# Performance work log

Hardware: AMD Instinct MI355X
Metric: run time of the kernel (lower is better)

## Reference

```python
import math
import jax, jax.numpy as jnp
import numpy as np

B, L, T, D, H, SD = 8, 512, 512, 768, 12, 5


def setup_inputs() -> dict:
    key = jax.random.key(0)
    ks = jax.random.split(key, 16)
    s = 0.02
    return {
        "q": jax.random.normal(ks[0], (B, L, D), jnp.float32),
        "k": jax.random.normal(ks[1], (B, T, D), jnp.float32),
        "v": jax.random.normal(ks[2], (B, T, D), jnp.float32),
        "pairwise_locs": jax.random.normal(ks[3], (B, L, T, SD), jnp.float32),
        "key_padding_mask": jax.random.randint(ks[4], (B, T), 0, 2).astype(bool),
        "Wq": jax.random.normal(ks[5], (D, D), jnp.float32) * s,
        "bq": jnp.zeros((D,), jnp.float32),
        "Wk": jax.random.normal(ks[6], (D, D), jnp.float32) * s,
        "bk": jnp.zeros((D,), jnp.float32),
        "Wv": jax.random.normal(ks[7], (D, D), jnp.float32) * s,
        "bv": jnp.zeros((D,), jnp.float32),
        "Wl": jax.random.normal(ks[8], (D, H * (SD + 1)), jnp.float32) * s,
        "bl": jnp.zeros((H * (SD + 1),), jnp.float32),
        "Wf": jax.random.normal(ks[9], (D, D), jnp.float32) * s,
        "bf": jnp.zeros((D,), jnp.float32),
    }


def reference(q, k, v, pairwise_locs, key_padding_mask,
              Wq, bq, Wk, bk, Wv, bv, Wl, bl, Wf, bf):
    b, l, d = q.shape
    t = k.shape[1]
    sd = pairwise_locs.shape[-1]
    h = Wl.shape[1] // (sd + 1)          # spatial_multihead=True -> h == n_head
    dh = d // h

    # projections -> [h, b, seq, dh]
    qh = (q @ Wq + bq).reshape(b, l, h, dh).transpose(2, 0, 1, 3)
    kh = (k @ Wk + bk).reshape(b, t, h, dh).transpose(2, 0, 1, 3)
    vh = (v @ Wv + bv).reshape(b, t, h, dh).transpose(2, 0, 1, 3)

    attn = jnp.einsum('hblk,hbtk->hblt', qh, kh) / math.sqrt(dh)

    # language-conditioned spatial weights from residual (= q input)
    sw = (q @ Wl + bl).reshape(b, l, h, sd + 1).transpose(2, 0, 1, 3)  # [h,b,l,sd+1]
    spatial_bias = sw[..., :1]
    spatial_w = sw[..., 1:]
    loc_attn = jax.nn.sigmoid(
        jnp.einsum('hbld,bltd->hblt', spatial_w, pairwise_locs) + spatial_bias)

    mask = key_padding_mask[None, :, None, :]          # [1,b,1,t]
    attn = jnp.where(mask, -jnp.inf, attn)
    loc_attn = jnp.where(mask, 0.0, loc_attn)

    fused_attn = jax.nn.softmax(jnp.log(jnp.clip(loc_attn, 1e-6)) + attn, axis=3)

    out = jnp.einsum('hblt,hbtv->hblv', fused_attn, vh)
    out = out.transpose(1, 2, 0, 3).reshape(b, l, d)
    out = out @ Wf + bf
    return (out, fused_attn)
```

## Files before the change

kernel.cpp:

```cpp
#include <hip/hip_runtime.h>
#include <hip/hip_bf16.h>

#define B_ 8
#define L_ 512
#define T_ 512
#define D_ 768
#define H_ 12
#define DH_ 64
#define SD_ 5
#define NSW_ 72
#define K2_ 1536
#define K3_ 2304

typedef __attribute__((ext_vector_type(8))) short bf16x8;
typedef __attribute__((ext_vector_type(4))) float f32x4;
typedef unsigned short ushort_t;

__device__ __forceinline__ unsigned short f2bf(float x) {
    union { __hip_bfloat16 h; unsigned short u; } cv;
    cv.h = __float2bfloat16(x);
    return cv.u;
}
__device__ __forceinline__ float bf2f(unsigned short u) {
    union { unsigned short u; __hip_bfloat16 h; } cv;
    cv.u = u;
    return __bfloat162float(cv.h);
}

__device__ __forceinline__ void gload_lds16(const void* g, void* l) {
    __builtin_amdgcn_global_load_lds((const __attribute__((address_space(1))) void*)g,
                                     (__attribute__((address_space(3))) void*)l,
                                     16, 0, 0);
}

__global__ __launch_bounds__(256) void asplit_kernel(
    const float* __restrict__ q, const float* __restrict__ k, const float* __restrict__ v,
    short* __restrict__ q2, short* __restrict__ k2, short* __restrict__ v2)
{
    const int z = blockIdx.z;
    const float* A = (z == 0) ? q : (z == 1) ? k : v;
    short* O = (z == 0) ? q2 : (z == 1) ? k2 : v2;
    const int col = blockIdx.x * 256 + threadIdx.x;
    const int m   = blockIdx.y;
    if (col >= D_) return;
    const float a = A[(size_t)m * D_ + col];
    const unsigned short hi = f2bf(a);
    const unsigned short lo = f2bf(a - bf2f(hi));
    O[(size_t)m * K2_ + col]       = (short)hi;
    O[(size_t)m * K2_ + D_ + col]  = (short)lo;
}

__global__ __launch_bounds__(256) void wsplit_kernel(
    const float* __restrict__ Wq, const float* __restrict__ Wk,
    const float* __restrict__ Wv, const float* __restrict__ Wl,
    const float* __restrict__ Wf,
    short* __restrict__ WqT3, short* __restrict__ WkT3, short* __restrict__ WvT3,
    short* __restrict__ WlT3, short* __restrict__ WfT3)
{
    const int z = blockIdx.z;
    const float* W; short* O; int Nw, Npad;
    if (z == 0)      { W = Wq; O = WqT3; Nw = D_;   Npad = 768; }
    else if (z == 1) { W = Wk; O = WkT3; Nw = D_;   Npad = 768; }
    else if (z == 2) { W = Wv; O = WvT3; Nw = D_;   Npad = 768; }
    else if (z == 3) { W = Wl; O = WlT3; Nw = NSW_; Npad = 128; }
    else             { W = Wf; O = WfT3; Nw = D_;   Npad = 768; }

    const int k0 = blockIdx.x * 64;
    const int n0 = blockIdx.y * 64;
    if (n0 >= Npad) return;

    __shared__ float sm[64][65];
    const int c  = threadIdx.x & 63;
    const int r4 = threadIdx.x >> 6;

#pragma unroll
    for (int i = 0; i < 16; i++) {
        const int r = i * 4 + r4;
        float val = 0.f;
        if (n0 + c < Nw) val = W[(size_t)(k0 + r) * Nw + n0 + c];
        sm[r][c] = val;
    }
    __syncthreads();

#pragma unroll
    for (int i = 0; i < 16; i++) {
        const int nl = i * 4 + r4;
        const int n  = n0 + nl;
        if (n >= Npad) continue;
        const float v = (n < Nw) ? sm[c][nl] : 0.f;
        const unsigned short hi = f2bf(v);
        const unsigned short lo = f2bf(v - bf2f(hi));
        const size_t rb = (size_t)n * K3_;
        O[rb + k0 + c]        = (short)hi;
        O[rb + 768 + k0 + c]  = (short)lo;
        O[rb + 1536 + k0 + c] = (short)hi;
    }
}

__global__ __launch_bounds__(256) void mfma_gemm(
    const short* __restrict__ q2, const short* __restrict__ k2, const short* __restrict__ v2,
    const short* __restrict__ WqT3, const short* __restrict__ WkT3,
    const short* __restrict__ WvT3, const short* __restrict__ WlT3,
    const short* __restrict__ WfT3,
    const float* __restrict__ bq, const float* __restrict__ bk,
    const float* __restrict__ bv, const float* __restrict__ bl,
    const float* __restrict__ bf,
    const short* __restrict__ outp2,
    ushort_t* __restrict__ qs2a, ushort_t* __restrict__ ks2a, ushort_t* __restrict__ vt2,
    float* __restrict__ swv, float* __restrict__ outf,
    int zoff)
{
    const int z = zoff + blockIdx.z;
    const short* A2; const short* WT3; const float* bias;
    if (z == 0)      { A2 = q2;    WT3 = WqT3; bias = bq; }
    else if (z == 1) { A2 = k2;    WT3 = WkT3; bias = bk; }
    else if (z == 2) { A2 = v2;    WT3 = WvT3; bias = bv; }
    else if (z == 3) { A2 = q2;    WT3 = WlT3; bias = bl; }
    else             { A2 = outp2; WT3 = WfT3; bias = bf; }

    if (z == 3 && blockIdx.x != 0) return;

    const int m0 = blockIdx.y * 128;
    const int n0 = blockIdx.x * 128;

    __shared__ __align__(16) short As[128 * 32];
    __shared__ __align__(16) short Bs[128 * 32];

    const int tid  = threadIdx.x;
    const int lane = tid & 63;
    const int wv_  = tid >> 6;
    const int wm   = (wv_ & 1) << 6;
    const int wn   = (wv_ >> 1) << 6;
    const int l15  = lane & 15;
    const int quad = lane >> 4;

    f32x4 acc[4][4] = {};

    const int sa  = tid;
    const int sb  = tid + 256;
    const int ra  = sa >> 2, ka = (sa & 3) << 3;
    const int rb  = sb >> 2, kb8 = (sb & 3) << 3;

    for (int kb = 0; kb < K3_; kb += 32) {
        const int akb = (kb < 768) ? kb : kb - 768;
        __syncthreads();
        gload_lds16(A2  + (size_t)(m0 + ra) * K2_ + akb + ka,  &As[sa << 3]);
        gload_lds16(A2  + (size_t)(m0 + rb) * K2_ + akb + kb8, &As[sb << 3]);
        gload_lds16(WT3 + (size_t)(n0 + ra) * K3_ + kb  + ka,  &Bs[sa << 3]);
        gload_lds16(WT3 + (size_t)(n0 + rb) * K3_ + kb  + kb8, &Bs[sb << 3]);
        __syncthreads();

        bf16x8 af[4], bfr[4];
#pragma unroll
        for (int t = 0; t < 4; t++) {
            af[t]  = *(const bf16x8*)&As[(wm + t * 16 + l15) * 32 + quad * 8];
            bfr[t] = *(const bf16x8*)&Bs[(wn + t * 16 + l15) * 32 + quad * 8];
        }
#pragma unroll
        for (int mt = 0; mt < 4; mt++)
#pragma unroll
            for (int nt = 0; nt < 4; nt++)
                acc[mt][nt] = __builtin_amdgcn_mfma_f32_16x16x32_bf16(
                    af[mt], bfr[nt], acc[mt][nt], 0, 0, 0);
    }

    if (z <= 2) {
        ushort_t* dst = (z == 0) ? qs2a : (z == 1) ? ks2a : vt2;
#pragma unroll
        for (int nt = 0; nt < 4; nt++) {
            const int col = n0 + wn + nt * 16 + l15;
            const int hh = col >> 6, dd = col & 63;
            const float bvv = bias[col];
#pragma unroll
            for (int mt = 0; mt < 4; mt++) {
                const int rowb = m0 + wm + mt * 16 + quad * 4;
                if (z < 2) {
#pragma unroll
                    for (int r = 0; r < 4; r++) {
                        const int gr = rowb + r;
                        const int bb = gr >> 9, ll = gr & 511;
                        const float x = acc[mt][nt][r] + bvv;
                        const ushort_t hi = f2bf(x);
                        const ushort_t lo = f2bf(x - bf2f(hi));
                        const size_t base = (((size_t)hh * B_ + bb) * 512 + ll) * 128 + dd;
                        dst[base]      = hi;
                        dst[base + 64] = lo;
                    }
                } else {
                    const int bb = rowb >> 9, tt = rowb & 511;
                    ushort_t hi4[4], lo4[4];
#pragma unroll
                    for (int r = 0; r < 4; r++) {
                        const float x = acc[mt][nt][r] + bvv;
                        hi4[r] = f2bf(x);
                        lo4[r] = f2bf(x - bf2f(hi4[r]));
                    }
                    const size_t base = (((size_t)hh * B_ + bb) * 128 + dd) * 512 + tt;
                    *(ushort4*)&dst[base]            = *(ushort4*)hi4;
                    *(ushort4*)&dst[base + 64 * 512] = *(ushort4*)lo4;
                }
            }
        }
    } else if (z == 3) {
#pragma unroll
        for (int nt = 0; nt < 4; nt++) {
            const int col = n0 + wn + nt * 16 + l15;
            if (col >= NSW_) continue;
            const float bvv = bias[col];
#pragma unroll
            for (int mt = 0; mt < 4; mt++) {
                const int row = m0 + wm + mt * 16 + quad * 4;
#pragma unroll
                for (int r = 0; r < 4; r++)
                    swv[(size_t)(row + r) * NSW_ + col] = acc[mt][nt][r] + bvv;
            }
        }
    } else {
#pragma unroll
        for (int nt = 0; nt < 4; nt++) {
            const int col = n0 + wn + nt * 16 + l15;
            const float bvv = bias[col];
#pragma unroll
            for (int mt = 0; mt < 4; mt++) {
                const int row = m0 + wm + mt * 16 + quad * 4;
#pragma unroll
                for (int r = 0; r < 4; r++)
                    outf[(size_t)(row + r) * D_ + col] = acc[mt][nt][r] + bvv;
            }
        }
    }
}

__global__ __launch_bounds__(256) void sig_kernel(
    const float* __restrict__ ploc, const float* __restrict__ swv,
    const int* __restrict__ maskp, _Float16* __restrict__ sig16)
{
    const int b = blockIdx.y;
    const int l = blockIdx.x;
    const int tid = threadIdx.x;

    __shared__ float pls[512 * 5];
    __shared__ float sws[72];
    __shared__ int   msk[512];

    const float* src = ploc + (size_t)(b * 512 + l) * 512 * 5;
    for (int i = tid; i < 640; i += 256)
        *(float4*)&pls[i * 4] = *(const float4*)(src + i * 4);
    if (tid < 72) sws[tid] = swv[(size_t)(b * 512 + l) * NSW_ + tid];
    for (int i = tid; i < 512; i += 256) msk[i] = maskp[b * 512 + i];
    __syncthreads();

    for (int e = tid; e < H_ * 512; e += 256) {
        const int t  = e & 511;
        const int hh = e >> 9;
        float s = sws[hh * 6];
#pragma unroll
        for (int d = 0; d < SD_; d++) s += sws[hh * 6 + 1 + d] * pls[t * 5 + d];
        const float sig = msk[t] ? 0.f : fmaxf(1.f / (1.f + __expf(-s)), 1e-6f);
        sig16[(((size_t)hh * B_ + b) * 512 + l) * 512 + t] = (_Float16)sig;
    }
}

__global__ __launch_bounds__(256) void attn_kernel(
    const ushort_t* __restrict__ qs2, const ushort_t* __restrict__ ks2,
    const ushort_t* __restrict__ vt2, const _Float16* __restrict__ sig16,
    float* __restrict__ fused, ushort_t* __restrict__ outp2,
    float* __restrict__ sums)
{
    const int h  = blockIdx.z;
    const int b  = blockIdx.y;
    const int l0 = blockIdx.x << 6;
    const int hb = h * B_ + b;
    const int tid  = threadIdx.x;
    const int lane = tid & 63;
    const int wv   = tid >> 6;
    const int l15  = lane & 15;
    const int quad = lane >> 4;

    __shared__ __align__(16) ushort_t qs[64 * 128];
    __shared__ __align__(16) ushort_t ks[64 * 128];
    __shared__ __align__(16) ushort_t vts[128 * 64];
    __shared__ __align__(16) ushort_t ps[64 * 136];
    __shared__ float ssb[4 * 64];
    __shared__ float ssum[64];

    {
        const size_t qbase = ((size_t)hb * 512 + l0) * 128;
#pragma unroll
        for (int j = 0; j < 4; j++) {
            const int i = tid + 256 * j;
            const int r = i >> 4, c = i & 15, gc = c ^ (r & 7);
            gload_lds16(qs2 + qbase + r * 128 + gc * 8, &qs[i * 8]);
        }
    }

    float pacc = 0.f;
    f32x4 accpv[4] = {};

    for (int t0 = 0; t0 < T_; t0 += 64) {
        __syncthreads();
        {
            const size_t kbase = ((size_t)hb * 512 + t0) * 128;
#pragma unroll
            for (int j = 0; j < 4; j++) {
                const int i = tid + 256 * j;
                const int r = i >> 4, c = i & 15, gc = c ^ (r & 7);
                gload_lds16(ks2 + kbase + r * 128 + gc * 8, &ks[i * 8]);
            }
            const size_t vbase = (size_t)hb * 128 * 512;
#pragma unroll
            for (int j = 0; j < 4; j++) {
                const int i = tid + 256 * j;
                const int r = i >> 3, c = i & 7, gc = c ^ (r & 7);
                gload_lds16(vt2 + vbase + (size_t)r * 512 + t0 + gc * 8, &vts[i * 8]);
            }
        }
        __syncthreads();

        float sigv[4][4];
        {
            const _Float16* sgp = sig16 + (((size_t)hb * 512 + l0) * 512) + t0 + wv * 16 + l15;
#pragma unroll
            for (int mt = 0; mt < 4; mt++)
#pragma unroll
                for (int r2 = 0; r2 < 4; r2++)
                    sigv[mt][r2] = (float)sgp[(size_t)(mt * 16 + quad * 4 + r2) * 512];
        }

        f32x4 acq[4] = {};
        {
            const int trow = wv * 16 + l15;
            const int tsw  = trow & 7;
            const bf16x8 bk0 = *(const bf16x8*)&ks[trow * 128 + ((0  + quad) ^ tsw) * 8];
            const bf16x8 bk1 = *(const bf16x8*)&ks[trow * 128 + ((4  + quad) ^ tsw) * 8];
            const bf16x8 bk2 = *(const bf16x8*)&ks[trow * 128 + ((8  + quad) ^ tsw) * 8];
            const bf16x8 bk3 = *(const bf16x8*)&ks[trow * 128 + ((12 + quad) ^ tsw) * 8];
#pragma unroll
            for (int mt = 0; mt < 4; mt++) {
                const int arow = mt * 16 + l15;
                const int asw  = arow & 7;
                const bf16x8 a0 = *(const bf16x8*)&qs[arow * 128 + ((0  + quad) ^ asw) * 8];
                const bf16x8 a1 = *(const bf16x8*)&qs[arow * 128 + ((4  + quad) ^ asw) * 8];
                const bf16x8 a2 = *(const bf16x8*)&qs[arow * 128 + ((8  + quad) ^ asw) * 8];
                const bf16x8 a3 = *(const bf16x8*)&qs[arow * 128 + ((12 + quad) ^ asw) * 8];
                f32x4 a = acq[mt];
                a = __builtin_amdgcn_mfma_f32_16x16x32_bf16(a0, bk0, a, 0, 0, 0);
                a = __builtin_amdgcn_mfma_f32_16x16x32_bf16(a1, bk1, a, 0, 0, 0);
                a = __builtin_amdgcn_mfma_f32_16x16x32_bf16(a0, bk2, a, 0, 0, 0);
                a = __builtin_amdgcn_mfma_f32_16x16x32_bf16(a1, bk3, a, 0, 0, 0);
                a = __builtin_amdgcn_mfma_f32_16x16x32_bf16(a2, bk0, a, 0, 0, 0);
                a = __builtin_amdgcn_mfma_f32_16x16x32_bf16(a3, bk1, a, 0, 0, 0);
                acq[mt] = a;
            }
        }

        {
            const int tcol = wv * 16 + l15;
#pragma unroll
            for (int mt = 0; mt < 4; mt++)
#pragma unroll
                for (int r2 = 0; r2 < 4; r2++) {
                    const int lrow = mt * 16 + quad * 4 + r2;
                    const float p  = sigv[mt][r2] * __expf(acq[mt][r2] * 0.125f);
                    const ushort_t hi = f2bf(p);
                    const ushort_t lo = f2bf(p - bf2f(hi));
                    ps[lrow * 136 + tcol]      = hi;
                    ps[lrow * 136 + 64 + tcol] = lo;
                }
        }
        __syncthreads();

        {
            const int row = tid >> 2, c4 = tid & 3;
            float vbuf[16];
            float s = 0.f;
#pragma unroll
            for (int jj = 0; jj < 16; jj++) {
                const int t = c4 * 16 + jj;
                const float pv = bf2f(ps[row * 136 + t]) + bf2f(ps[row * 136 + 64 + t]);
                vbuf[jj] = pv;
                s += pv;
            }
            pacc += s;
            float* dstf = fused + ((size_t)hb * 512 + l0 + row) * 512 + t0 + c4 * 16;
#pragma unroll
            for (int jj = 0; jj < 4; jj++)
                *(float4*)(dstf + jj * 4) = *(float4*)&vbuf[jj * 4];
        }

        {
            const int vrh = wv * 16 + l15;
            const int vrl = 64 + vrh;
            const int swh = vrh & 7, swl = vrl & 7;
            const bf16x8 bh0 = *(const bf16x8*)&vts[vrh * 64 + ((0 + quad) ^ swh) * 8];
            const bf16x8 bh1 = *(const bf16x8*)&vts[vrh * 64 + ((4 + quad) ^ swh) * 8];
            const bf16x8 bl0 = *(const bf16x8*)&vts[vrl * 64 + ((0 + quad) ^ swl) * 8];
            const bf16x8 bl1 = *(const bf16x8*)&vts[vrl * 64 + ((4 + quad) ^ swl) * 8];
#pragma unroll
            for (int mt = 0; mt < 4; mt++) {
                const int prow = mt * 16 + l15;
                const bf16x8 ph0 = *(const bf16x8*)&ps[prow * 136 + 0  + quad * 8];
                const bf16x8 ph1 = *(const bf16x8*)&ps[prow * 136 + 32 + quad * 8];
                const bf16x8 pl0 = *(const bf16x8*)&ps[prow * 136 + 64 + quad * 8];
                const bf16x8 pl1 = *(const bf16x8*)&ps[prow * 136 + 96 + quad * 8];
                f32x4 a = accpv[mt];
                a = __builtin_amdgcn_mfma_f32_16x16x32_bf16(ph0, bh0, a, 0, 0, 0);
                a = __builtin_amdgcn_mfma_f32_16x16x32_bf16(ph1, bh1, a, 0, 0, 0);
                a = __builtin_amdgcn_mfma_f32_16x16x32_bf16(ph0, bl0, a, 0, 0, 0);
                a = __builtin_amdgcn_mfma_f32_16x16x32_bf16(ph1, bl1, a, 0, 0, 0);
                a = __builtin_amdgcn_mfma_f32_16x16x32_bf16(pl0, bh0, a, 0, 0, 0);
                a = __builtin_amdgcn_mfma_f32_16x16x32_bf16(pl1, bh1, a, 0, 0, 0);
                accpv[mt] = a;
            }
        }
    }

    __syncthreads();
    ssb[(tid & 3) * 64 + (tid >> 2)] = pacc;
    __syncthreads();
    if (tid < 64) {
        const float s = ssb[tid] + ssb[64 + tid] + ssb[128 + tid] + ssb[192 + tid];
        ssum[tid] = s;
        sums[(size_t)hb * 512 + l0 + tid] = s;
    }
    __syncthreads();

#pragma unroll
    for (int mt = 0; mt < 4; mt++)
#pragma unroll
        for (int r2 = 0; r2 < 4; r2++) {
            const int lrow = mt * 16 + quad * 4 + r2;
            const float val = accpv[mt][r2] / ssum[lrow];
            const ushort_t hi = f2bf(val);
            const ushort_t lo = f2bf(val - bf2f(hi));
            const size_t obase = ((size_t)(b * 512 + l0 + lrow)) * K2_ + h * 64 + wv * 16 + l15;
            outp2[obase]       = hi;
            outp2[obase + D_]  = lo;
        }
}

__global__ __launch_bounds__(256) void norm_kernel(
    float* __restrict__ fused, const float* __restrict__ sums)
{
    const int gi = blockIdx.x * 256 + threadIdx.x;
    float4* f4 = (float4*)fused;
    float4 v = f4[gi];
    const float inv = 1.f / sums[gi >> 7];
    v.x *= inv; v.y *= inv; v.z *= inv; v.w *= inv;
    f4[gi] = v;
}

extern "C" void kernel_launch(void* const* d_in, const int* in_sizes, int n_in,
                              void* d_out, int out_size, void* d_ws, size_t ws_size,
                              hipStream_t stream) {
    const float* q    = (const float*)d_in[0];
    const float* k    = (const float*)d_in[1];
    const float* v    = (const float*)d_in[2];
    const float* ploc = (const float*)d_in[3];
    const int*   mask = (const int*)  d_in[4];
    const float* Wq   = (const float*)d_in[5];
    const float* bq   = (const float*)d_in[6];
    const float* Wk   = (const float*)d_in[7];
    const float* bk   = (const float*)d_in[8];
    const float* Wv   = (const float*)d_in[9];
    const float* bv   = (const float*)d_in[10];
    const float* Wl   = (const float*)d_in[11];
    const float* bl   = (const float*)d_in[12];
    const float* Wf   = (const float*)d_in[13];
    const float* bf   = (const float*)d_in[14];

    char* base = (char*)d_ws;
    short*    q2    = (short*)(base + 0);
    short*    k2    = (short*)(base + 12582912);
    short*    v2    = (short*)(base + 25165824);
    short*    WqT3  = (short*)(base + 37748736);
    short*    WkT3  = (short*)(base + 41287680);
    short*    WvT3  = (short*)(base + 44826624);
    short*    WlT3  = (short*)(base + 48365568);
    _Float16* sig16 = (_Float16*)(base + 0);
    short*    WfT3  = (short*)(base + 50331648);
    ushort_t* qs2a  = (ushort_t*)(base + 53870592);
    ushort_t* ks2a  = (ushort_t*)(base + 66453504);
    ushort_t* vt2   = (ushort_t*)(base + 79036416);
    float*    swv   = (float*)(base + 91619328);
    float*    sums  = (float*)(base + 92798976);
    short*    outp2 = (short*)(base + 92995584);

    float* out   = (float*)d_out;
    float* fused = out + (size_t)4096 * D_;

    asplit_kernel<<<dim3(3, 4096, 3), 256, 0, stream>>>(q, k, v, q2, k2, v2);
    wsplit_kernel<<<dim3(12, 12, 5), 256, 0, stream>>>(
        Wq, Wk, Wv, Wl, Wf, WqT3, WkT3, WvT3, WlT3, WfT3);

    mfma_gemm<<<dim3(6, 32, 4), 256, 0, stream>>>(
        q2, k2, v2, WqT3, WkT3, WvT3, WlT3, WfT3,
        bq, bk, bv, bl, bf, outp2, qs2a, ks2a, vt2, swv, out, 0);

    sig_kernel<<<dim3(512, 8), 256, 0, stream>>>(ploc, swv, mask, sig16);

    attn_kernel<<<dim3(8, 8, 12), 256, 0, stream>>>(
        qs2a, ks2a, vt2, sig16, fused, (ushort_t*)outp2, sums);

    norm_kernel<<<dim3(24576), 256, 0, stream>>>(fused, sums);

    mfma_gemm<<<dim3(6, 32, 1), 256, 0, stream>>>(
        q2, k2, v2, WqT3, WkT3, WvT3, WlT3, WfT3,
        bq, bk, bv, bl, bf, outp2, qs2a, ks2a, vt2, swv, out, 4);
}
```

Measured before the change: 517.6 us.

## Widen GEMM K-tile to 64 with XOR-swizzled LDS and XCD-aware block remapping

The projection GEMM now stages 64-wide K slices instead of 32, halving the number of barrier-synchronised load phases. The LDS layout uses an XOR swizzle on 16-byte chunks so fragment reads avoid bank conflicts. Both the GEMM and attention kernels remap the flat workgroup index so that consecutive logical tiles land on the same XCD, aiming to improve L2 reuse across the chiplets. LDS use doubles and the index arithmetic hard-codes the grid shape (6x32 tiles, an 8x8x12 attention grid), which breaks if the launch dimensions change.

```diff
diff --git a/kernel.cpp b/kernel.cpp
--- a/kernel.cpp
+++ b/kernel.cpp
@@ -110,7 +110,15 @@
     float* __restrict__ swv, float* __restrict__ outf,
     int zoff)
 {
-    const int z = zoff + blockIdx.z;
+    const int nwg   = gridDim.x * gridDim.y * gridDim.z;
+    const int flat  = blockIdx.x + gridDim.x * (blockIdx.y + gridDim.y * blockIdx.z);
+    const int flat2 = (flat & 7) * (nwg >> 3) + (flat >> 3);
+    const int bxg   = flat2 % 6;
+    const int rem   = flat2 / 6;
+    const int byg   = rem & 31;
+    const int bzg   = rem >> 5;
+
+    const int z = zoff + bzg;
     const short* A2; const short* WT3; const float* bias;
     if (z == 0)      { A2 = q2;    WT3 = WqT3; bias = bq; }
     else if (z == 1) { A2 = k2;    WT3 = WkT3; bias = bk; }
@@ -118,13 +126,13 @@
     else if (z == 3) { A2 = q2;    WT3 = WlT3; bias = bl; }
     else             { A2 = outp2; WT3 = WfT3; bias = bf; }
 
-    if (z == 3 && blockIdx.x != 0) return;
-
-    const int m0 = blockIdx.y * 128;
-    const int n0 = blockIdx.x * 128;
-
-    __shared__ __align__(16) short As[128 * 32];
-    __shared__ __align__(16) short Bs[128 * 32];
+    if (z == 3 && bxg != 0) return;
+
+    const int m0 = byg * 128;
+    const int n0 = bxg * 128;
+
+    __shared__ __align__(16) short As[128 * 64];
+    __shared__ __align__(16) short Bs[128 * 64];
 
     const int tid  = threadIdx.x;
     const int lane = tid & 63;
@@ -136,32 +144,40 @@
 
     f32x4 acc[4][4] = {};
 
-    const int sa  = tid;
-    const int sb  = tid + 256;
-    const int ra  = sa >> 2, ka = (sa & 3) << 3;
-    const int rb  = sb >> 2, kb8 = (sb & 3) << 3;
-
-    for (int kb = 0; kb < K3_; kb += 32) {
+    for (int kb = 0; kb < K3_; kb += 64) {
         const int akb = (kb < 768) ? kb : kb - 768;
         __syncthreads();
-        gload_lds16(A2  + (size_t)(m0 + ra) * K2_ + akb + ka,  &As[sa << 3]);
-        gload_lds16(A2  + (size_t)(m0 + rb) * K2_ + akb + kb8, &As[sb << 3]);
-        gload_lds16(WT3 + (size_t)(n0 + ra) * K3_ + kb  + ka,  &Bs[sa << 3]);
-        gload_lds16(WT3 + (size_t)(n0 + rb) * K3_ + kb  + kb8, &Bs[sb << 3]);
+#pragma unroll
+        for (int j = 0; j < 4; j++) {
+            const int i = tid + 256 * j;
+            const int r = i >> 3, c = i & 7, gc = c ^ (r & 7);
+            gload_lds16(A2 + (size_t)(m0 + r) * K2_ + akb + gc * 8, &As[i * 8]);
+        }
+#pragma unroll
+        for (int j = 0; j < 4; j++) {
+            const int i = tid + 256 * j;
+            const int r = i >> 3, c = i & 7, gc = c ^ (r & 7);
+            gload_lds16(WT3 + (size_t)(n0 + r) * K3_ + kb + gc * 8, &Bs[i * 8]);
+        }
         __syncthreads();
 
-        bf16x8 af[4], bfr[4];
-#pragma unroll
-        for (int t = 0; t < 4; t++) {
-            af[t]  = *(const bf16x8*)&As[(wm + t * 16 + l15) * 32 + quad * 8];
-            bfr[t] = *(const bf16x8*)&Bs[(wn + t * 16 + l15) * 32 + quad * 8];
-        }
-#pragma unroll
-        for (int mt = 0; mt < 4; mt++)
-#pragma unroll
-            for (int nt = 0; nt < 4; nt++)
-                acc[mt][nt] = __builtin_amdgcn_mfma_f32_16x16x32_bf16(
-                    af[mt], bfr[nt], acc[mt][nt], 0, 0, 0);
+#pragma unroll
+        for (int kk = 0; kk < 2; kk++) {
+            bf16x8 af[4], bfr[4];
+#pragma unroll
+            for (int t = 0; t < 4; t++) {
+                const int ar = wm + t * 16 + l15;
+                const int br = wn + t * 16 + l15;
+                af[t]  = *(const bf16x8*)&As[ar * 64 + (((kk << 2) + quad) ^ (ar & 7)) * 8];
+                bfr[t] = *(const bf16x8*)&Bs[br * 64 + (((kk << 2) + quad) ^ (br & 7)) * 8];
+            }
+#pragma unroll
+            for (int mt = 0; mt < 4; mt++)
+#pragma unroll
+                for (int nt = 0; nt < 4; nt++)
+                    acc[mt][nt] = __builtin_amdgcn_mfma_f32_16x16x32_bf16(
+                        af[mt], bfr[nt], acc[mt][nt], 0, 0, 0);
+        }
     }
 
     if (z <= 2) {
@@ -267,9 +283,12 @@
     float* __restrict__ fused, ushort_t* __restrict__ outp2,
     float* __restrict__ sums)
 {
-    const int h  = blockIdx.z;
-    const int b  = blockIdx.y;
-    const int l0 = blockIdx.x << 6;
+    const int flat  = blockIdx.x + 8 * (blockIdx.y + 8 * blockIdx.z);
+    const int flat2 = (flat & 7) * 96 + (flat >> 3);
+    const int h  = flat2 / 64;
+    const int b  = (flat2 >> 3) & 7;
+    const int l0 = (flat2 & 7) << 6;
+
     const int hb = h * B_ + b;
     const int tid  = threadIdx.x;
     const int lane = tid & 63;
```

Result: faster. 483.6 us (-6.6%).
